# Kernel optimization log

Measured on AMD Instinct MI355X. Metric: run time of the kernel, lower is better.

## Reference

```python
import jax, jax.numpy as jnp
import numpy as np

B, T, C, H, S, M = 4, 4096, 1024, 16, 256, 32
D = C // H  # size_head = 64


def setup_inputs() -> dict:
    key = jax.random.key(0)
    ks = jax.random.split(key, 10)
    scale = 1.0 / (C * C)
    return {
        "x_q": jax.random.normal(ks[0], (B, T, C), dtype=jnp.float32),
        "x_r": jax.random.normal(ks[1], (B, T, C), dtype=jnp.float32),
        "y": jax.random.normal(ks[2], (B, T, C), dtype=jnp.float32),
        "Wi": jax.random.normal(ks[3], (C, C), dtype=jnp.float32) * 0.02,
        "bi": jnp.zeros((C,), jnp.float32),
        "Ws": jax.random.normal(ks[4], (S, D), dtype=jnp.float32) * 0.02,
        "bs": jnp.zeros((S,), jnp.float32),
        "temp": jnp.ones((1, H, 1, 1), jnp.float32) / jnp.sqrt(jnp.float32(D)),
        "w_re": jax.random.uniform(ks[5], (H, D, D, M), dtype=jnp.float32) * scale,
        "w_im": jax.random.uniform(ks[6], (H, D, D, M), dtype=jnp.float32) * scale,
        "Wo": jax.random.normal(ks[7], (C, C), dtype=jnp.float32) * 0.02,
        "bo": jnp.zeros((C,), jnp.float32),
    }


def reference(x_q, x_r, y, Wi, bi, Ws, bs, temp, w_re, w_im, Wo, bo):
    b, t, c = x_q.shape
    d = c // H
    # in_proj -> [B, H, T, D]
    tmp = (x_q @ Wi.T + bi).reshape(b, t, H, d).transpose(0, 2, 1, 3)
    # slice logits [B, H, T, S], scaled by learned temperature
    logits = (tmp @ Ws.T + bs) / temp
    # softmax over tokens (n): slice-attention pooling to S virtual points
    z = jnp.einsum('bhnc,bhns->bhsc', tmp, jax.nn.softmax(logits, axis=-2))
    z = z.transpose(0, 1, 3, 2)  # [B, H, D, S]
    n = z.shape[-1]
    z_fft = jnp.fft.rfft(z)  # [B, H, D, S//2+1]
    w = (w_re + 1j * w_im).astype(z_fft.dtype)
    out_m = jnp.einsum('bhix,hiox->bhox', z_fft[..., :M], w)  # [B, H, D, M]
    out_ft = jnp.zeros((b, H, d, n // 2 + 1), dtype=out_m.dtype).at[..., :M].set(out_m)
    out = jnp.fft.irfft(out_ft, n=n)  # [B, H, D, S]
    out = out.transpose(0, 1, 3, 2)  # [B, H, S, D]
    # softmax over slices (g): scatter back to tokens
    out = jnp.einsum('bhgc,bhng->bhnc', out, jax.nn.softmax(logits, axis=-1))
    out = out.transpose(0, 2, 1, 3).reshape(b, t, c)  # merge heads
    return out @ Wo.T + bo
```

## Files before the change

kernel.cpp:

```cpp
#include <hip/hip_runtime.h>
#include <hip/hip_bf16.h>

typedef __attribute__((ext_vector_type(8))) _Float16 half8;
typedef __attribute__((ext_vector_type(4))) _Float16 half4;
typedef __attribute__((ext_vector_type(4))) float f32x4;

#define DEVFN __device__ __forceinline__

constexpr int B_ = 4, T_ = 4096, C_ = 1024, H_ = 16, S_ = 256, M_ = 32, D_ = 64;
constexpr int NT_ = B_ * T_;
constexpr float FSCALE = 65536.0f;
constexpr float TWOPI = 6.283185307179586f;

DEVFN half8 cvt8(const float4 a, const float4 b) {
  half8 h;
  h[0] = (_Float16)a.x; h[1] = (_Float16)a.y; h[2] = (_Float16)a.z; h[3] = (_Float16)a.w;
  h[4] = (_Float16)b.x; h[5] = (_Float16)b.y; h[6] = (_Float16)b.z; h[7] = (_Float16)b.w;
  return h;
}

#define GLD16(gsrc, ldst)                                                        \
  __builtin_amdgcn_global_load_lds(                                              \
      (const __attribute__((address_space(1))) uint32_t*)(gsrc),                 \
      (__attribute__((address_space(3))) uint32_t*)(ldst), 16, 0, 0)

__global__ void k_diag(float* __restrict__ out, float wsz) {
  if (threadIdx.x == 0 && blockIdx.x == 0) out[0] = wsz;
}

__global__ void kw_cvt(const float* __restrict__ src, _Float16* __restrict__ dst, int n) {
  const int i = (blockIdx.x * blockDim.x + threadIdx.x) * 8;
  if (i < n) {
    float4 a = ((const float4*)(src + i))[0];
    float4 b = ((const float4*)(src + i))[1];
    *(half8*)(dst + i) = cvt8(a, b);
  }
}

__global__ void k0_prep(const float* __restrict__ Ws, const float* __restrict__ bs,
                        const float* __restrict__ temp,
                        _Float16* __restrict__ Wsh, float* __restrict__ bsh) {
  const int h = blockIdx.x;
  const int tid = threadIdx.x;
  const float invt = 1.0f / temp[h];
  for (int i = tid; i < S_ * D_; i += 256)
    Wsh[(size_t)h * S_ * D_ + i] = (_Float16)(Ws[i] * invt);
  if (tid < S_) bsh[h * S_ + tid] = bs[tid] * invt;
}

__global__ __launch_bounds__(256) void k1_in_proj(
    const _Float16* __restrict__ Xh, const _Float16* __restrict__ Wih, const float* __restrict__ bi,
    _Float16* __restrict__ tmp_h)
{
  __shared__ _Float16 As[128 * 32];
  __shared__ _Float16 Bs[128 * 32];
  const int tid = threadIdx.x;
  const int orig = blockIdx.y * gridDim.x + blockIdx.x;
  const int wgid = (orig & 7) * 128 + (orig >> 3);
  const int rowBase = (wgid >> 3) * 128;
  const int colBase = (wgid & 7) * 128;
  const int w = tid >> 6, lane = tid & 63;
  const int wr = w >> 1, wc = w & 1;
  const int fr = lane & 15, fg = lane >> 4;
  const int srow0 = w * 16 + (lane >> 2);
  const int srow1 = (4 + w) * 16 + (lane >> 2);
  const int scol  = (lane & 3) * 8;
  const size_t arow0 = (size_t)(rowBase + srow0) * C_ + scol;
  const size_t arow1 = (size_t)(rowBase + srow1) * C_ + scol;
  const size_t brow0 = (size_t)(colBase + srow0) * C_ + scol;
  const size_t brow1 = (size_t)(colBase + srow1) * C_ + scol;
  f32x4 acc[4][4] = {};
  for (int kt = 0; kt < C_; kt += 32) {
    __syncthreads();
    GLD16(Xh  + arow0 + kt, &As[w * 512]);
    GLD16(Xh  + arow1 + kt, &As[(4 + w) * 512]);
    GLD16(Wih + brow0 + kt, &Bs[w * 512]);
    GLD16(Wih + brow1 + kt, &Bs[(4 + w) * 512]);
    __syncthreads();
    half8 a[4], b[4];
#pragma unroll
    for (int i = 0; i < 4; ++i) a[i] = *(const half8*)&As[(wr * 64 + i * 16 + fr) * 32 + fg * 8];
#pragma unroll
    for (int j = 0; j < 4; ++j) b[j] = *(const half8*)&Bs[(wc * 64 + j * 16 + fr) * 32 + fg * 8];
#pragma unroll
    for (int i = 0; i < 4; ++i)
#pragma unroll
      for (int j = 0; j < 4; ++j)
        acc[i][j] = __builtin_amdgcn_mfma_f32_16x16x32_f16(a[i], b[j], acc[i][j], 0, 0, 0);
  }
#pragma unroll
  for (int i = 0; i < 4; ++i) {
#pragma unroll
    for (int j = 0; j < 4; ++j) {
      const int col = colBase + wc * 64 + j * 16 + fr;
      const int hh = col >> 6, d = col & 63;
      const float bv = bi[col];
      const int g0 = rowBase + wr * 64 + i * 16 + fg * 4;
#pragma unroll
      for (int r = 0; r < 4; ++r) {
        const int g = g0 + r;
        const int bb = g >> 12;
        const int t = g & (T_ - 1);
        tmp_h[(((size_t)(bb * H_ + hh)) * T_ + t) * D_ + d] = (_Float16)(acc[i][j][r] + bv);
      }
    }
  }
}

__global__ __launch_bounds__(256) void k3_pool(
    const _Float16* __restrict__ tmp_h, const _Float16* __restrict__ Wsh,
    const float* __restrict__ bsh,
    float* __restrict__ Zpart, float* __restrict__ rowsum, float* __restrict__ colsumP)
{
  __shared__ _Float16 Es[256][72];
  __shared__ _Float16 Bt[64][72];
  __shared__ float red[64][4];
  const int tid = threadIdx.x;
  const int kc = blockIdx.x;
  const int bh = blockIdx.y;
  const int hh = bh & (H_ - 1);
  const int w = tid >> 6, lane = tid & 63;
  const int fr = lane & 15, fg = lane >> 4;
  const size_t tmpB = (size_t)bh * T_ * D_;
  const _Float16* WshH = Wsh + (size_t)hh * S_ * D_;
  float bsreg[4];
#pragma unroll
  for (int nj = 0; nj < 4; ++nj) bsreg[nj] = bsh[hh * S_ + w * 64 + nj * 16 + fr];
  f32x4 acc2[4][4] = {};
  float cacc[4] = {0.f, 0.f, 0.f, 0.f};
  for (int step = 0; step < 16; ++step) {
    const int t0 = kc * 1024 + step * 64;
    {
      const int tl = tid >> 2, cc = (tid & 3) * 16;
      const _Float16* src = tmp_h + tmpB + (size_t)(t0 + tl) * D_ + cc;
      half8 v0 = ((const half8*)src)[0];
      half8 v1 = ((const half8*)src)[1];
#pragma unroll
      for (int k2 = 0; k2 < 8; ++k2) Bt[cc + k2][tl] = v0[k2];
#pragma unroll
      for (int k2 = 0; k2 < 8; ++k2) Bt[cc + 8 + k2][tl] = v1[k2];
    }
    f32x4 acc1[4][4] = {};
#pragma unroll
    for (int ks = 0; ks < 2; ++ks) {
      half8 a[4], b[4];
#pragma unroll
      for (int mi = 0; mi < 4; ++mi)
        a[mi] = *(const half8*)(tmp_h + tmpB + (size_t)(t0 + mi * 16 + fr) * D_ + ks * 32 + fg * 8);
#pragma unroll
      for (int nj = 0; nj < 4; ++nj)
        b[nj] = *(const half8*)(WshH + (size_t)(w * 64 + nj * 16 + fr) * D_ + ks * 32 + fg * 8);
#pragma unroll
      for (int mi = 0; mi < 4; ++mi)
#pragma unroll
        for (int nj = 0; nj < 4; ++nj)
          acc1[mi][nj] = __builtin_amdgcn_mfma_f32_16x16x32_f16(a[mi], b[nj], acc1[mi][nj], 0, 0, 0);
    }
#pragma unroll
    for (int mi = 0; mi < 4; ++mi) {
      float rsp[4] = {0.f, 0.f, 0.f, 0.f};
#pragma unroll
      for (int nj = 0; nj < 4; ++nj) {
        half4 p;
        float csp = 0.f;
#pragma unroll
        for (int r = 0; r < 4; ++r) {
          const float e = __expf(acc1[mi][nj][r] + bsreg[nj]);
          p[r] = (_Float16)e;
          rsp[r] += e;
          csp += e;
        }
        cacc[nj] += csp;
        *(half4*)&Es[w * 64 + nj * 16 + fr][mi * 16 + fg * 4] = p;
      }
#pragma unroll
      for (int r = 0; r < 4; ++r) {
        float v = rsp[r];
        v += __shfl_xor(v, 1); v += __shfl_xor(v, 2);
        v += __shfl_xor(v, 4); v += __shfl_xor(v, 8);
        if (fr == 0) red[mi * 16 + fg * 4 + r][w] = v;
      }
    }
    __syncthreads();
#pragma unroll
    for (int kt = 0; kt < 2; ++kt) {
      half8 a2[4], b2[4];
#pragma unroll
      for (int mi = 0; mi < 4; ++mi) a2[mi] = *(const half8*)&Es[w * 64 + mi * 16 + fr][kt * 32 + fg * 8];
#pragma unroll
      for (int nj = 0; nj < 4; ++nj) b2[nj] = *(const half8*)&Bt[nj * 16 + fr][kt * 32 + fg * 8];
#pragma unroll
      for (int mi = 0; mi < 4; ++mi)
#pragma unroll
        for (int nj = 0; nj < 4; ++nj)
          acc2[mi][nj] = __builtin_amdgcn_mfma_f32_16x16x32_f16(a2[mi], b2[nj], acc2[mi][nj], 0, 0, 0);
    }
    if (tid < 64)
      rowsum[(size_t)bh * T_ + t0 + tid] = red[tid][0] + red[tid][1] + red[tid][2] + red[tid][3];
    __syncthreads();
  }
#pragma unroll
  for (int nj = 0; nj < 4; ++nj) {
    float v = cacc[nj];
    v += __shfl_xor(v, 16); v += __shfl_xor(v, 32);
    if (fg == 0) colsumP[((size_t)bh * 4 + kc) * S_ + w * 64 + nj * 16 + fr] = v;
  }
#pragma unroll
  for (int mi = 0; mi < 4; ++mi)
#pragma unroll
    for (int nj = 0; nj < 4; ++nj)
#pragma unroll
      for (int r = 0; r < 4; ++r)
        Zpart[(((size_t)bh * 4 + kc) * S_ + w * 64 + mi * 16 + fg * 4 + r) * D_ + nj * 16 + fr]
            = acc2[mi][nj][r];
}

__global__ __launch_bounds__(256) void k4a_dft(
    const float* __restrict__ Zpart, const float* __restrict__ colsumP,
    float* __restrict__ Fre, float* __restrict__ Fim)
{
  __shared__ float zsh[256][17];
  __shared__ float csh[256];
  __shared__ float tc[256], ts[256];
  const int tid = threadIdx.x;
  const int ic = blockIdx.x;
  const int bh = blockIdx.y;
  {
    const float ang = (float)tid * (TWOPI / 256.0f);
    tc[tid] = cosf(ang); ts[tid] = sinf(ang);
    float c = 0.f;
#pragma unroll
    for (int kc = 0; kc < 4; ++kc) c += colsumP[((size_t)bh * 4 + kc) * S_ + tid];
    csh[tid] = c;
  }
  __syncthreads();
  for (int idx = tid; idx < 256 * 16; idx += 256) {
    const int s = idx >> 4, dd = idx & 15;
    float v = 0.f;
#pragma unroll
    for (int kc = 0; kc < 4; ++kc)
      v += Zpart[(((size_t)bh * 4 + kc) * S_ + s) * D_ + ic * 16 + dd];
    zsh[s][dd] = v / csh[s];
  }
  __syncthreads();
  const int ii = tid >> 4;
  const int mh = tid & 15;
#pragma unroll
  for (int q = 0; q < 2; ++q) {
    const int m = mh + 16 * q;
    float re = 0.f, im = 0.f;
    int k = 0;
    for (int s = 0; s < 256; ++s) {
      const float zv = zsh[s][ii];
      re += zv * tc[k];
      im -= zv * ts[k];
      k = (k + m) & 255;
    }
    Fre[((size_t)bh * D_ + ic * 16 + ii) * M_ + m] = re;
    Fim[((size_t)bh * D_ + ic * 16 + ii) * M_ + m] = im;
  }
}

__global__ __launch_bounds__(256) void k4b_mix(
    const float* __restrict__ Fre, const float* __restrict__ Fim,
    const float* __restrict__ w_re, const float* __restrict__ w_im,
    _Float16* __restrict__ fout_T)
{
  __shared__ _Float16 Fsr[4][64][33];
  __shared__ _Float16 Fsi[4][64][33];
  __shared__ float Gpre[2][4][4][32];
  __shared__ float Gpim[2][4][4][32];
  __shared__ float Gre[4][4][32];
  __shared__ float Gim[4][4][32];
  __shared__ float tc[256], ts[256];
  const int tid = threadIdx.x;
  const int oc = blockIdx.x;
  const int h  = blockIdx.y;
  for (int idx = tid; idx < 4 * 64 * 32; idx += 256) {
    const int b = idx >> 11, rem = idx & 2047, i = rem >> 5, m = rem & 31;
    const size_t off = ((size_t)(b * 16 + h) * D_ + i) * M_ + m;
    Fsr[b][i][m] = (_Float16)Fre[off];
    Fsi[b][i][m] = (_Float16)Fim[off];
  }
  {
    const float ang = (float)tid * (TWOPI / 256.0f);
    tc[tid] = cosf(ang); ts[tid] = sinf(ang);
  }
  __syncthreads();
  {
    const int ih = tid >> 7, o = (tid >> 5) & 3, m = tid & 31;
    float gre[4] = {0,0,0,0}, gim[4] = {0,0,0,0};
    for (int i = ih * 32; i < ih * 32 + 32; ++i) {
      const size_t wo = (((size_t)h * D_ + i) * D_ + oc * 4 + o) * M_ + m;
      const float wre = w_re[wo], wim = w_im[wo];
#pragma unroll
      for (int b = 0; b < 4; ++b) {
        const float fre = (float)Fsr[b][i][m], fim = (float)Fsi[b][i][m];
        gre[b] += fre * wre - fim * wim;
        gim[b] += fre * wim + fim * wre;
      }
    }
#pragma unroll
    for (int b = 0; b < 4; ++b) { Gpre[ih][b][o][m] = gre[b]; Gpim[ih][b][o][m] = gim[b]; }
  }
  __syncthreads();
  for (int idx = tid; idx < 512; idx += 256) {
    const int b = idx >> 7, o = (idx >> 5) & 3, m = idx & 31;
    Gre[b][o][m] = Gpre[0][b][o][m] + Gpre[1][b][o][m];
    Gim[b][o][m] = Gpim[0][b][o][m] + Gpim[1][b][o][m];
  }
  __syncthreads();
  {
    const int b = tid >> 6, o = (tid >> 4) & 3, sc = tid & 15;
    for (int s5 = 0; s5 < 16; ++s5) {
      const int s = sc * 16 + s5;
      float v = Gre[b][o][0];
      int km = s;
#pragma unroll
      for (int m = 1; m < 32; ++m) {
        v += 2.0f * (Gre[b][o][m] * tc[km] - Gim[b][o][m] * ts[km]);
        km = (km + s) & 255;
      }
      fout_T[((size_t)(b * 16 + h) * D_ + oc * 4 + o) * S_ + s] = (_Float16)(v * (FSCALE / 256.0f));
    }
  }
}

__global__ __launch_bounds__(256) void k5_scatter(
    const _Float16* __restrict__ Wsh, const float* __restrict__ bsh,
    const _Float16* __restrict__ fout_T, const float* __restrict__ rowsum,
    _Float16* __restrict__ tmp_io)
{
  __shared__ _Float16 Fs[64][264];
  __shared__ _Float16 Es[64][264];
  __shared__ float bshl[256];
  const int tid = threadIdx.x;
  const int orig = blockIdx.y * gridDim.x + blockIdx.x;
  const int nidx = (orig & 7) * 64 + (orig >> 3);
  const int bh = nidx >> 3;
  const int tcn = nidx & 7;
  const int hh = bh & (H_ - 1);
  const int w = tid >> 6, lane = tid & 63;
  const int fr = lane & 15, fg = lane >> 4;
  {
    const int row = tid >> 2, c0 = (tid & 3) * 64;
    const _Float16* src = fout_T + (size_t)bh * D_ * S_ + (size_t)row * S_ + c0;
#pragma unroll
    for (int q = 0; q < 8; ++q)
      *(half8*)&Fs[row][c0 + q * 8] = ((const half8*)src)[q];
  }
  bshl[tid] = bsh[hh * S_ + tid];
  __syncthreads();
  const _Float16* WshH = Wsh + (size_t)hh * S_ * D_;
  const size_t tmpB = (size_t)bh * T_ * D_ + (size_t)tcn * 512 * D_;
  const int trow = w * 16 + fr;
  half8 bf0, bf1;
  {
    const _Float16* p = tmp_io + tmpB + (size_t)trow * D_ + fg * 8;
    bf0 = *(const half8*)p;
    bf1 = *(const half8*)(p + 32);
  }
  for (int step = 0; step < 8; ++step) {
    {
      f32x4 acc1[8];
#pragma unroll
      for (int mi = 0; mi < 8; ++mi) acc1[mi] = (f32x4){0.f, 0.f, 0.f, 0.f};
#pragma unroll
      for (int mi = 0; mi < 8; ++mi) {
        const half8 a0 = *(const half8*)(WshH + (size_t)(mi * 16 + fr) * D_ + fg * 8);
        acc1[mi] = __builtin_amdgcn_mfma_f32_16x16x32_f16(a0, bf0, acc1[mi], 0, 0, 0);
      }
#pragma unroll
      for (int mi = 0; mi < 8; ++mi) {
        const half8 a1 = *(const half8*)(WshH + (size_t)(mi * 16 + fr) * D_ + 32 + fg * 8);
        acc1[mi] = __builtin_amdgcn_mfma_f32_16x16x32_f16(a1, bf1, acc1[mi], 0, 0, 0);
      }
#pragma unroll
      for (int mi = 0; mi < 8; ++mi) {
        const float4 bv = *(const float4*)&bshl[mi * 16 + fg * 4];
        half4 pk;
        pk[0] = (_Float16)__expf(acc1[mi][0] + bv.x);
        pk[1] = (_Float16)__expf(acc1[mi][1] + bv.y);
        pk[2] = (_Float16)__expf(acc1[mi][2] + bv.z);
        pk[3] = (_Float16)__expf(acc1[mi][3] + bv.w);
        *(half4*)&Es[trow][mi * 16 + fg * 4] = pk;
      }
    }
    {
      f32x4 acc1[8];
#pragma unroll
      for (int mi = 0; mi < 8; ++mi) acc1[mi] = (f32x4){0.f, 0.f, 0.f, 0.f};
#pragma unroll
      for (int mi = 0; mi < 8; ++mi) {
        const half8 a0 = *(const half8*)(WshH + (size_t)((8 + mi) * 16 + fr) * D_ + fg * 8);
        acc1[mi] = __builtin_amdgcn_mfma_f32_16x16x32_f16(a0, bf0, acc1[mi], 0, 0, 0);
      }
#pragma unroll
      for (int mi = 0; mi < 8; ++mi) {
        const half8 a1 = *(const half8*)(WshH + (size_t)((8 + mi) * 16 + fr) * D_ + 32 + fg * 8);
        acc1[mi] = __builtin_amdgcn_mfma_f32_16x16x32_f16(a1, bf1, acc1[mi], 0, 0, 0);
      }
#pragma unroll
      for (int mi = 0; mi < 8; ++mi) {
        const float4 bv = *(const float4*)&bshl[(8 + mi) * 16 + fg * 4];
        half4 pk;
        pk[0] = (_Float16)__expf(acc1[mi][0] + bv.x);
        pk[1] = (_Float16)__expf(acc1[mi][1] + bv.y);
        pk[2] = (_Float16)__expf(acc1[mi][2] + bv.z);
        pk[3] = (_Float16)__expf(acc1[mi][3] + bv.w);
        *(half4*)&Es[trow][(8 + mi) * 16 + fg * 4] = pk;
      }
    }
    if (step < 7) {
      const _Float16* p = tmp_io + tmpB + (size_t)((step + 1) * 64 + trow) * D_ + fg * 8;
      bf0 = *(const half8*)p;
      bf1 = *(const half8*)(p + 32);
    }
    f32x4 acc2[4];
#pragma unroll
    for (int nj = 0; nj < 4; ++nj) acc2[nj] = (f32x4){0.f, 0.f, 0.f, 0.f};
#pragma unroll
    for (int ks = 0; ks < 8; ++ks) {
      const half8 ea = *(const half8*)&Es[w * 16 + fr][ks * 32 + fg * 8];
#pragma unroll
      for (int nj = 0; nj < 4; ++nj) {
        const half8 fb = *(const half8*)&Fs[nj * 16 + fr][ks * 32 + fg * 8];
        acc2[nj] = __builtin_amdgcn_mfma_f32_16x16x32_f16(ea, fb, acc2[nj], 0, 0, 0);
      }
    }
    const int tbase = tcn * 512 + step * 64 + w * 16 + fg * 4;
    const float4 rs = *(const float4*)&rowsum[(size_t)bh * T_ + tbase];
    const float ri[4] = {1.0f / rs.x, 1.0f / rs.y, 1.0f / rs.z, 1.0f / rs.w};
#pragma unroll
    for (int r = 0; r < 4; ++r) {
      _Float16* dst = tmp_io + (size_t)bh * T_ * D_ + (size_t)(tbase + r) * D_ + fr;
#pragma unroll
      for (int nj = 0; nj < 4; ++nj)
        dst[nj * 16] = (_Float16)(acc2[nj][r] * ri[r]);
    }
  }
}

__global__ __launch_bounds__(256) void k6_out_proj(
    const _Float16* __restrict__ OT, const _Float16* __restrict__ Woh, const float* __restrict__ bo,
    float* __restrict__ Y)
{
  __shared__ _Float16 As[128 * 32];
  __shared__ _Float16 Bs[128 * 32];
  const int tid = threadIdx.x;
  const int orig = blockIdx.y * gridDim.x + blockIdx.x;
  const int wgid = (orig & 7) * 128 + (orig >> 3);
  const int rowBase = (wgid >> 3) * 128;
  const int colBase = (wgid & 7) * 128;
  const int w = tid >> 6, lane = tid & 63;
  const int wr = w >> 1, wc = w & 1;
  const int fr = lane & 15, fg = lane >> 4;
  const int srow0 = w * 16 + (lane >> 2);
  const int srow1 = (4 + w) * 16 + (lane >> 2);
  const int scol  = (lane & 3) * 8;
  const int g0 = rowBase + srow0, g1 = rowBase + srow1;
  const int bb = g0 >> 12;
  const int t0 = g0 & (T_ - 1), t1 = g1 & (T_ - 1);
  const size_t brow0 = (size_t)(colBase + srow0) * C_ + scol;
  const size_t brow1 = (size_t)(colBase + srow1) * C_ + scol;
  f32x4 acc[4][4] = {};
  for (int kt = 0; kt < C_; kt += 32) {
    const int c0 = kt + scol;
    const int hh0 = c0 >> 6, d0 = c0 & 63;
    __syncthreads();
    GLD16(OT + (((size_t)(bb * H_ + hh0)) * T_ + t0) * D_ + d0, &As[w * 512]);
    GLD16(OT + (((size_t)(bb * H_ + hh0)) * T_ + t1) * D_ + d0, &As[(4 + w) * 512]);
    GLD16(Woh + brow0 + kt, &Bs[w * 512]);
    GLD16(Woh + brow1 + kt, &Bs[(4 + w) * 512]);
    __syncthreads();
    half8 a[4], b[4];
#pragma unroll
    for (int i = 0; i < 4; ++i) a[i] = *(const half8*)&As[(wr * 64 + i * 16 + fr) * 32 + fg * 8];
#pragma unroll
    for (int j = 0; j < 4; ++j) b[j] = *(const half8*)&Bs[(wc * 64 + j * 16 + fr) * 32 + fg * 8];
#pragma unroll
    for (int i = 0; i < 4; ++i)
#pragma unroll
      for (int j = 0; j < 4; ++j)
        acc[i][j] = __builtin_amdgcn_mfma_f32_16x16x32_f16(a[i], b[j], acc[i][j], 0, 0, 0);
  }
#pragma unroll
  for (int i = 0; i < 4; ++i) {
#pragma unroll
    for (int j = 0; j < 4; ++j) {
      const int col = colBase + wc * 64 + j * 16 + fr;
      const float bv = bo[col];
      const int g0o = rowBase + wr * 64 + i * 16 + fg * 4;
#pragma unroll
      for (int r = 0; r < 4; ++r)
        Y[(size_t)(g0o + r) * C_ + col] = acc[i][j][r] * (1.0f / FSCALE) + bv;
    }
  }
}

extern "C" void kernel_launch(void* const* d_in, const int* in_sizes, int n_in,
                              void* d_out, int out_size, void* d_ws, size_t ws_size,
                              hipStream_t stream)
{
  const float* x_q  = (const float*)d_in[0];
  const float* Wi   = (const float*)d_in[3];
  const float* bi   = (const float*)d_in[4];
  const float* Ws   = (const float*)d_in[5];
  const float* bs   = (const float*)d_in[6];
  const float* temp = (const float*)d_in[7];
  const float* w_re = (const float*)d_in[8];
  const float* w_im = (const float*)d_in[9];
  const float* Wo   = (const float*)d_in[10];
  const float* bo   = (const float*)d_in[11];
  float* Y = (float*)d_out;

  char* ws = (char*)d_ws;
  size_t off = 0;
  auto alloc = [&](size_t bytes) { size_t o = off; off += (bytes + 255) & ~(size_t)255; return o; };
  const size_t o_tmp  = alloc((size_t)NT_ * C_ * 2);
  const size_t o_Wsh  = alloc((size_t)H_ * S_ * D_ * 2);
  const size_t o_bsh  = alloc((size_t)H_ * S_ * 4);
  const size_t o_Zp   = alloc((size_t)B_ * H_ * 4 * S_ * D_ * 4);
  const size_t o_row  = alloc((size_t)B_ * H_ * T_ * 4);
  const size_t o_colP = alloc((size_t)B_ * H_ * 4 * S_ * 4);
  const size_t o_Fre  = alloc((size_t)B_ * H_ * D_ * M_ * 4);
  const size_t o_Fim  = alloc((size_t)B_ * H_ * D_ * M_ * 4);
  const size_t o_fout = alloc((size_t)B_ * H_ * D_ * S_ * 2);
  const size_t o_Wih  = alloc((size_t)C_ * C_ * 2);
  const size_t o_Woh  = alloc((size_t)C_ * C_ * 2);
  if (off > ws_size) {
    k_diag<<<1, 64, 0, stream>>>(Y, (float)ws_size);
    return;
  }

  _Float16* tmp    = (_Float16*)(ws + o_tmp);
  _Float16* Wsh    = (_Float16*)(ws + o_Wsh);
  float*    bsh    = (float*)(ws + o_bsh);
  float*    Zpart  = (float*)(ws + o_Zp);
  float*    rowsum = (float*)(ws + o_row);
  float*    colsumP= (float*)(ws + o_colP);
  float*    Fre    = (float*)(ws + o_Fre);
  float*    Fim    = (float*)(ws + o_Fim);
  _Float16* fout_T = (_Float16*)(ws + o_fout);
  _Float16* Wih    = (_Float16*)(ws + o_Wih);
  _Float16* Woh    = (_Float16*)(ws + o_Woh);
  _Float16* Xh     = (_Float16*)d_out;

  kw_cvt    <<<dim3(8192),    256, 0, stream>>>(x_q, Xh, NT_ * C_);
  kw_cvt    <<<dim3(512),     256, 0, stream>>>(Wi, Wih, C_ * C_);
  kw_cvt    <<<dim3(512),     256, 0, stream>>>(Wo, Woh, C_ * C_);
  k0_prep   <<<dim3(H_),      256, 0, stream>>>(Ws, bs, temp, Wsh, bsh);
  k1_in_proj<<<dim3(8, 128),  256, 0, stream>>>(Xh, Wih, bi, tmp);
  k3_pool   <<<dim3(4, B_*H_), 256, 0, stream>>>(tmp, Wsh, bsh, Zpart, rowsum, colsumP);
  k4a_dft   <<<dim3(4, B_*H_), 256, 0, stream>>>(Zpart, colsumP, Fre, Fim);
  k4b_mix   <<<dim3(16, H_),   256, 0, stream>>>(Fre, Fim, w_re, w_im, fout_T);
  k5_scatter<<<dim3(8, B_*H_), 256, 0, stream>>>(Wsh, bsh, fout_T, rowsum, tmp);
  k6_out_proj<<<dim3(8, 128),  256, 0, stream>>>(tmp, Woh, bo, Y);
}
```

Baseline: 312.0 us.

## Emit transposed tmp copy from in_proj and double pooling split-K parallelism

The in-projection epilogue now also writes a head-major transposed copy of tmp (D x T per head), so the pooling kernel can load its B tile with vector loads instead of scattered element-wise LDS transposes. The pooling kernel also splits the token dimension into 8 chunks instead of 4, doubling grid size, and the DFT kernel reduces 8 partials. This adds an extra 32 MB of half-precision writes in in_proj and more partial-sum traffic. The transposed buffer is placed in the output buffer region after the X half copy.

```diff
diff --git a/kernel.cpp b/kernel.cpp
--- a/kernel.cpp
+++ b/kernel.cpp
@@ -50,7 +50,7 @@
 
 __global__ __launch_bounds__(256) void k1_in_proj(
     const _Float16* __restrict__ Xh, const _Float16* __restrict__ Wih, const float* __restrict__ bi,
-    _Float16* __restrict__ tmp_h)
+    _Float16* __restrict__ tmp_h, _Float16* __restrict__ tmp_hT)
 {
   __shared__ _Float16 As[128 * 32];
   __shared__ _Float16 Bs[128 * 32];
@@ -96,20 +96,23 @@
       const int hh = col >> 6, d = col & 63;
       const float bv = bi[col];
       const int g0 = rowBase + wr * 64 + i * 16 + fg * 4;
+      const int bb = g0 >> 12;
+      const int t0 = g0 & (T_ - 1);
+      half4 pk;
 #pragma unroll
       for (int r = 0; r < 4; ++r) {
-        const int g = g0 + r;
-        const int bb = g >> 12;
-        const int t = g & (T_ - 1);
-        tmp_h[(((size_t)(bb * H_ + hh)) * T_ + t) * D_ + d] = (_Float16)(acc[i][j][r] + bv);
-      }
+        const _Float16 hv = (_Float16)(acc[i][j][r] + bv);
+        tmp_h[(((size_t)(bb * H_ + hh)) * T_ + t0 + r) * D_ + d] = hv;
+        pk[r] = hv;
+      }
+      *(half4*)&tmp_hT[(((size_t)(bb * H_ + hh)) * D_ + d) * T_ + t0] = pk;
     }
   }
 }
 
 __global__ __launch_bounds__(256) void k3_pool(
-    const _Float16* __restrict__ tmp_h, const _Float16* __restrict__ Wsh,
-    const float* __restrict__ bsh,
+    const _Float16* __restrict__ tmp_h, const _Float16* __restrict__ tmp_hT,
+    const _Float16* __restrict__ Wsh, const float* __restrict__ bsh,
     float* __restrict__ Zpart, float* __restrict__ rowsum, float* __restrict__ colsumP)
 {
   __shared__ _Float16 Es[256][72];
@@ -121,24 +124,21 @@
   const int hh = bh & (H_ - 1);
   const int w = tid >> 6, lane = tid & 63;
   const int fr = lane & 15, fg = lane >> 4;
-  const size_t tmpB = (size_t)bh * T_ * D_;
+  const size_t tmpB  = (size_t)bh * T_ * D_;
+  const size_t tmpTB = (size_t)bh * D_ * T_;
   const _Float16* WshH = Wsh + (size_t)hh * S_ * D_;
   float bsreg[4];
 #pragma unroll
   for (int nj = 0; nj < 4; ++nj) bsreg[nj] = bsh[hh * S_ + w * 64 + nj * 16 + fr];
   f32x4 acc2[4][4] = {};
   float cacc[4] = {0.f, 0.f, 0.f, 0.f};
-  for (int step = 0; step < 16; ++step) {
-    const int t0 = kc * 1024 + step * 64;
+  const int brow = tid >> 2, bc0 = (tid & 3) * 16;
+  for (int step = 0; step < 8; ++step) {
+    const int t0 = kc * 512 + step * 64;
     {
-      const int tl = tid >> 2, cc = (tid & 3) * 16;
-      const _Float16* src = tmp_h + tmpB + (size_t)(t0 + tl) * D_ + cc;
-      half8 v0 = ((const half8*)src)[0];
-      half8 v1 = ((const half8*)src)[1];
-#pragma unroll
-      for (int k2 = 0; k2 < 8; ++k2) Bt[cc + k2][tl] = v0[k2];
-#pragma unroll
-      for (int k2 = 0; k2 < 8; ++k2) Bt[cc + 8 + k2][tl] = v1[k2];
+      const _Float16* src = tmp_hT + tmpTB + (size_t)brow * T_ + t0 + bc0;
+      *(half8*)&Bt[brow][bc0]     = ((const half8*)src)[0];
+      *(half8*)&Bt[brow][bc0 + 8] = ((const half8*)src)[1];
     }
     f32x4 acc1[4][4] = {};
 #pragma unroll
@@ -203,7 +203,7 @@
   for (int nj = 0; nj < 4; ++nj) {
     float v = cacc[nj];
     v += __shfl_xor(v, 16); v += __shfl_xor(v, 32);
-    if (fg == 0) colsumP[((size_t)bh * 4 + kc) * S_ + w * 64 + nj * 16 + fr] = v;
+    if (fg == 0) colsumP[((size_t)bh * 8 + kc) * S_ + w * 64 + nj * 16 + fr] = v;
   }
 #pragma unroll
   for (int mi = 0; mi < 4; ++mi)
@@ -211,7 +211,7 @@
     for (int nj = 0; nj < 4; ++nj)
 #pragma unroll
       for (int r = 0; r < 4; ++r)
-        Zpart[(((size_t)bh * 4 + kc) * S_ + w * 64 + mi * 16 + fg * 4 + r) * D_ + nj * 16 + fr]
+        Zpart[(((size_t)bh * 8 + kc) * S_ + w * 64 + mi * 16 + fg * 4 + r) * D_ + nj * 16 + fr]
             = acc2[mi][nj][r];
 }
 
@@ -230,7 +230,7 @@
     tc[tid] = cosf(ang); ts[tid] = sinf(ang);
     float c = 0.f;
 #pragma unroll
-    for (int kc = 0; kc < 4; ++kc) c += colsumP[((size_t)bh * 4 + kc) * S_ + tid];
+    for (int kc = 0; kc < 8; ++kc) c += colsumP[((size_t)bh * 8 + kc) * S_ + tid];
     csh[tid] = c;
   }
   __syncthreads();
@@ -238,8 +238,8 @@
     const int s = idx >> 4, dd = idx & 15;
     float v = 0.f;
 #pragma unroll
-    for (int kc = 0; kc < 4; ++kc)
-      v += Zpart[(((size_t)bh * 4 + kc) * S_ + s) * D_ + ic * 16 + dd];
+    for (int kc = 0; kc < 8; ++kc)
+      v += Zpart[(((size_t)bh * 8 + kc) * S_ + s) * D_ + ic * 16 + dd];
     zsh[s][dd] = v / csh[s];
   }
   __syncthreads();
@@ -520,9 +520,9 @@
   const size_t o_tmp  = alloc((size_t)NT_ * C_ * 2);
   const size_t o_Wsh  = alloc((size_t)H_ * S_ * D_ * 2);
   const size_t o_bsh  = alloc((size_t)H_ * S_ * 4);
-  const size_t o_Zp   = alloc((size_t)B_ * H_ * 4 * S_ * D_ * 4);
+  const size_t o_Zp   = alloc((size_t)B_ * H_ * 8 * S_ * D_ * 4);
   const size_t o_row  = alloc((size_t)B_ * H_ * T_ * 4);
-  const size_t o_colP = alloc((size_t)B_ * H_ * 4 * S_ * 4);
+  const size_t o_colP = alloc((size_t)B_ * H_ * 8 * S_ * 4);
   const size_t o_Fre  = alloc((size_t)B_ * H_ * D_ * M_ * 4);
   const size_t o_Fim  = alloc((size_t)B_ * H_ * D_ * M_ * 4);
   const size_t o_fout = alloc((size_t)B_ * H_ * D_ * S_ * 2);
@@ -545,13 +545,14 @@
   _Float16* Wih    = (_Float16*)(ws + o_Wih);
   _Float16* Woh    = (_Float16*)(ws + o_Woh);
   _Float16* Xh     = (_Float16*)d_out;
+  _Float16* tmp_hT = (_Float16*)((char*)d_out + (size_t)NT_ * C_ * 2);
 
   kw_cvt    <<<dim3(8192),    256, 0, stream>>>(x_q, Xh, NT_ * C_);
   kw_cvt    <<<dim3(512),     256, 0, stream>>>(Wi, Wih, C_ * C_);
   kw_cvt    <<<dim3(512),     256, 0, stream>>>(Wo, Woh, C_ * C_);
   k0_prep   <<<dim3(H_),      256, 0, stream>>>(Ws, bs, temp, Wsh, bsh);
-  k1_in_proj<<<dim3(8, 128),  256, 0, stream>>>(Xh, Wih, bi, tmp);
-  k3_pool   <<<dim3(4, B_*H_), 256, 0, stream>>>(tmp, Wsh, bsh, Zpart, rowsum, colsumP);
+  k1_in_proj<<<dim3(8, 128),  256, 0, stream>>>(Xh, Wih, bi, tmp, tmp_hT);
+  k3_pool   <<<dim3(8, B_*H_), 256, 0, stream>>>(tmp, tmp_hT, Wsh, bsh, Zpart, rowsum, colsumP);
   k4a_dft   <<<dim3(4, B_*H_), 256, 0, stream>>>(Zpart, colsumP, Fre, Fim);
   k4b_mix   <<<dim3(16, H_),   256, 0, stream>>>(Fre, Fim, w_re, w_im, fout_T);
   k5_scatter<<<dim3(8, B_*H_), 256, 0, stream>>>(Wsh, bsh, fout_T, rowsum, tmp);
```

After: 328.2 us. 1.05x slower.
